# Performance work log

Measured on AMD Instinct MI355X. Metric: run time of the kernel, lower is better.

## Reference

```python
import jax, jax.numpy as jnp
import numpy as np


def setup_inputs() -> dict:
    key = jax.random.key(0)
    k1, k2, k3 = jax.random.split(key, 3)
    l, p, m, n = 8, 1, 4096, 1024
    inp = jax.random.normal(k1, (l, p, m, n), dtype=jnp.float32)
    alpha = jax.random.uniform(k2, (1,), dtype=jnp.float32, minval=0.001, maxval=1.0)
    beta = jax.random.uniform(k3, (1,), dtype=jnp.float32, minval=0.001, maxval=1.0)
    return {"input": inp, "alpha": alpha, "beta": beta}


def reference(input, alpha, beta):
    # w[0] = 1; w[k] = w[k-1] + alpha / w[k-1] - beta * input[..., k-1]
    l, p, m, n = input.shape
    a = alpha[0]
    b = beta[0]
    # scan over the last axis: move it to leading axis; only first n-1 inputs drive the recurrence
    xs = jnp.moveaxis(input[..., : n - 1], -1, 0)  # (n-1, l, p, m)
    w0 = jnp.ones((l, p, m), dtype=input.dtype)

    def step(w, x):
        w_next = w + a / w - b * x
        return w_next, w_next

    _, ws = jax.lax.scan(step, w0, xs)  # (n-1, l, p, m)
    wm = jnp.concatenate([w0[None], ws], axis=0)  # (n, l, p, m)
    wm = jnp.moveaxis(wm, 0, -1)  # (l, p, m, n)
    return wm.reshape(l, m * n)  # valid because p == 1
```

## Files before the change

### kernel.cpp

```cpp
#include <hip/hip_runtime.h>


#define N_COLS 1024
#define NCHUNK 64
#define KIN 6

#define WAITVM(n) asm volatile("s_waitcnt vmcnt(" #n ")" ::: "memory")
#define WAITLGKM0() asm volatile("s_waitcnt lgkmcnt(0)" ::: "memory")
#define BARRIER() __builtin_amdgcn_s_barrier()

__device__ __forceinline__ float fdiv_rn_exact(float a, float w) {
    float d, n, r0, e, r1, q, e2, q1, e3, f, res;
    unsigned long long sj;
    asm volatile(
        "v_div_scale_f32 %[d], vcc, %[w], %[w], %[a]\n\t"
        "v_div_scale_f32 %[n], %[sj], %[a], %[w], %[a]\n\t"
        "v_rcp_f32 %[r0], %[d]\n\t"
        "s_nop 1\n\t"
        "v_fma_f32 %[e], -%[d], %[r0], 1.0\n\t"
        "v_fma_f32 %[r1], %[e], %[r0], %[r0]\n\t"
        "v_mul_f32 %[q], %[n], %[r1]\n\t"
        "v_fma_f32 %[e2], -%[d], %[q], %[n]\n\t"
        "v_fma_f32 %[q1], %[e2], %[r1], %[q]\n\t"
        "v_fma_f32 %[e3], -%[d], %[q1], %[n]\n\t"
        "v_div_fmas_f32 %[f], %[e3], %[r1], %[q1]\n\t"
        "v_div_fixup_f32 %[res], %[f], %[w], %[a]"
        : [d] "=&v"(d), [n] "=&v"(n), [r0] "=&v"(r0), [e] "=&v"(e),
          [r1] "=&v"(r1), [q] "=&v"(q), [e2] "=&v"(e2), [q1] "=&v"(q1),
          [e3] "=&v"(e3), [f] "=&v"(f), [res] "=v"(res), [sj] "=&s"(sj)
        : [a] "v"(a), [w] "v"(w)
        : "vcc");
    return res;
}

__device__ __forceinline__ float stepf(float w, float x, float a, float b) {
    return __fsub_rn(__fadd_rn(w, fdiv_rn_exact(a, w)), __fmul_rn(b, x));
}

__global__ __launch_bounds__(256) void DDK_77644418777662_kernel(
    const float* __restrict__ in, float* __restrict__ out,
    const float* __restrict__ alpha, const float* __restrict__ beta,
    int n_rows) {
    __shared__ float ibuf[KIN * 2048];
    __shared__ float obuf[2 * 2048];

    const int tid = threadIdx.x;
    const int wid = tid >> 6;
    const int lane = tid & 63;
    const int row_base = blockIdx.x * 128;
    if (row_base >= n_rows) return;

    const int t = lane >> 2;
    const int u = lane & 3;
    const int cg = u ^ ((t >> 1) & 3);

    if (wid == 2) {
        const float* src0 = in + (size_t)(row_base + t) * N_COLS + cg * 4;

#define STAGE_AT(S, C) do {                                                    \
    float* dst_ = ibuf + (S) * 2048;                                           \
    const float* s_ = src0 + (size_t)(C) * 16;                                 \
    _Pragma("unroll")                                                          \
    for (int q_ = 0; q_ < 8; ++q_) {                                           \
        __builtin_amdgcn_global_load_lds(                                      \
            (const __attribute__((address_space(1))) void*)(s_ + q_ * 16 * N_COLS), \
            (__attribute__((address_space(3))) void*)(dst_ + q_ * 256), 16, 0, 0);  \
    }                                                                          \
} while (0)

        WAITVM(0);
        STAGE_AT(0, 0); STAGE_AT(1, 1); STAGE_AT(2, 2);
        STAGE_AT(3, 3); STAGE_AT(4, 4);
        WAITVM(32);

        int slot = KIN - 1;
#pragma unroll 1
        for (int c = 0; c < NCHUNK; ++c) {
            BARRIER();
            if (c <= NCHUNK - KIN) {
                STAGE_AT(slot, c + KIN - 1);
                WAITVM(32);
                if (++slot == KIN) slot = 0;
            } else if (c == 59) { WAITVM(24); }
            else if (c == 60) { WAITVM(16); }
            else if (c == 61) { WAITVM(8); }
            else if (c == 62) { WAITVM(0); }
        }
        BARRIER();
#undef STAGE_AT

    } else if (wid == 3) {
        float* dst0 = out + (size_t)(row_base + t) * N_COLS + cg * 4;

#define STORE_CHUNK(C) do {                                                    \
    const float* ob_ = obuf + ((C) & 1) * 2048;                                \
    float4 v_[8];                                                              \
    _Pragma("unroll")                                                          \
    for (int q_ = 0; q_ < 8; ++q_)                                             \
        v_[q_] = *(const float4*)(ob_ + q_ * 256 + lane * 4);                  \
    WAITLGKM0();                                                               \
    _Pragma("unroll")                                                          \
    for (int q_ = 0; q_ < 8; ++q_)                                             \
        *(float4*)(dst0 + (size_t)q_ * 16 * N_COLS + (size_t)(C) * 16) = v_[q_]; \
} while (0)

#pragma unroll 1
        for (int c = 0; c < NCHUNK; ++c) {
            BARRIER();
            if (c >= 1) STORE_CHUNK(c - 1);
        }
        BARRIER();
        STORE_CHUNK(NCHUNK - 1);
#undef STORE_CHUNK

    } else {
        const float a = alpha[0];
        const float b = beta[0];

        const int r = (wid << 6) + lane;
        const int rq = r >> 4, rr = r & 15;
        const int s = (rr >> 1) & 3;
        const int off0 = rq * 256 + (rr * 4 + (0 ^ s)) * 4;
        const int off1 = rq * 256 + (rr * 4 + (1 ^ s)) * 4;
        const int off2 = rq * 256 + (rr * 4 + (2 ^ s)) * 4;
        const int off3 = rq * 256 + (rr * 4 + (3 ^ s)) * 4;

        float w = 1.0f;
        int rslot = 0;
#pragma unroll 1
        for (int c = 0; c < NCHUNK; ++c) {
            BARRIER();
            const float* ib = ibuf + rslot * 2048;
            float4 xa = *(const float4*)(ib + off0);
            float4 xb = *(const float4*)(ib + off1);
            float4 xc = *(const float4*)(ib + off2);
            float4 xd = *(const float4*)(ib + off3);
            float x[16] = {xa.x, xa.y, xa.z, xa.w, xb.x, xb.y, xb.z, xb.w,
                           xc.x, xc.y, xc.z, xc.w, xd.x, xd.y, xd.z, xd.w};
            float o[16];
            o[0] = w;
#pragma unroll
            for (int i = 1; i < 16; ++i) { w = stepf(w, x[i - 1], a, b); o[i] = w; }
            w = stepf(w, x[15], a, b);

            float* ob = obuf + (c & 1) * 2048;
            *(float4*)(ob + off0) = make_float4(o[0], o[1], o[2], o[3]);
            *(float4*)(ob + off1) = make_float4(o[4], o[5], o[6], o[7]);
            *(float4*)(ob + off2) = make_float4(o[8], o[9], o[10], o[11]);
            *(float4*)(ob + off3) = make_float4(o[12], o[13], o[14], o[15]);
            WAITLGKM0();

            if (++rslot == KIN) rslot = 0;
        }
        BARRIER();
    }
}

extern "C" void kernel_launch(void* const* d_in, const int* in_sizes, int n_in,
                              void* d_out, int out_size, void* d_ws, size_t ws_size,
                              hipStream_t stream) {
    const float* in = (const float*)d_in[0];
    const float* alpha = (const float*)d_in[1];
    const float* beta = (const float*)d_in[2];
    float* out = (float*)d_out;

    int total = in_sizes[0];
    int n_rows = total / N_COLS;

    dim3 grid(n_rows / 128);
    dim3 block(256);
    DDK_77644418777662_kernel<<<grid, block, 0, stream>>>(in, out, alpha, beta,
                                                          n_rows);
}
```

Baseline: 283.3 us.

## Halve rows per block and double chunk width with an 8-deep input ring

Each block now covers 64 rows with a single compute wave (192 threads) in place of 128 rows with two compute waves. Chunks along the scan axis grow from 16 to 32 columns, so there are half as many barrier-synchronised iterations per block, and the input ring deepens from 6 to 8 slots with swizzled LDS offsets to match. The grid doubles, which raises block-level parallelism on a latency-bound serial recurrence. In exchange each compute lane does a longer dependent chain per chunk, and LDS use per block rises, which may limit how many blocks fit on a CU.

```diff
diff --git a/kernel.cpp b/kernel.cpp
--- a/kernel.cpp
+++ b/kernel.cpp
@@ -2,8 +2,11 @@
 
 
 #define N_COLS 1024
-#define NCHUNK 64
-#define KIN 6
+#define DC 32
+#define NDC 32
+#define RING 8
+#define ROWS 64
+#define SLOTF 2048
 
 #define WAITVM(n) asm volatile("s_waitcnt vmcnt(" #n ")" ::: "memory")
 #define WAITLGKM0() asm volatile("s_waitcnt lgkmcnt(0)" ::: "memory")
@@ -37,63 +40,62 @@
     return __fsub_rn(__fadd_rn(w, fdiv_rn_exact(a, w)), __fmul_rn(b, x));
 }
 
-__global__ __launch_bounds__(256) void DDK_77644418777662_kernel(
+__global__ __launch_bounds__(192) void DDK_77644418777662_kernel(
     const float* __restrict__ in, float* __restrict__ out,
     const float* __restrict__ alpha, const float* __restrict__ beta,
     int n_rows) {
-    __shared__ float ibuf[KIN * 2048];
-    __shared__ float obuf[2 * 2048];
+    __shared__ float ibuf[RING * SLOTF];
+    __shared__ float obuf[2 * SLOTF];
 
     const int tid = threadIdx.x;
     const int wid = tid >> 6;
     const int lane = tid & 63;
-    const int row_base = blockIdx.x * 128;
+    const int row_base = blockIdx.x * ROWS;
     if (row_base >= n_rows) return;
 
-    const int t = lane >> 2;
-    const int u = lane & 3;
-    const int cg = u ^ ((t >> 1) & 3);
+    const int lr = lane >> 3;
+    const int cg = (lane & 7) ^ lr;
 
-    if (wid == 2) {
-        const float* src0 = in + (size_t)(row_base + t) * N_COLS + cg * 4;
+    if (wid == 1) {
+        const float* src0 = in + (size_t)(row_base + lr) * N_COLS + cg * 4;
 
 #define STAGE_AT(S, C) do {                                                    \
-    float* dst_ = ibuf + (S) * 2048;                                           \
-    const float* s_ = src0 + (size_t)(C) * 16;                                 \
+    float* dst_ = ibuf + (S) * SLOTF;                                          \
+    const float* s_ = src0 + (C) * DC;                                         \
     _Pragma("unroll")                                                          \
     for (int q_ = 0; q_ < 8; ++q_) {                                           \
         __builtin_amdgcn_global_load_lds(                                      \
-            (const __attribute__((address_space(1))) void*)(s_ + q_ * 16 * N_COLS), \
-            (__attribute__((address_space(3))) void*)(dst_ + q_ * 256), 16, 0, 0);  \
+            (const __attribute__((address_space(1))) void*)(s_ + (size_t)q_ * 8 * N_COLS), \
+            (__attribute__((address_space(3))) void*)(dst_ + q_ * 256), 16, 0, 0);         \
     }                                                                          \
 } while (0)
 
         WAITVM(0);
-        STAGE_AT(0, 0); STAGE_AT(1, 1); STAGE_AT(2, 2);
-        STAGE_AT(3, 3); STAGE_AT(4, 4);
-        WAITVM(32);
+        STAGE_AT(0, 0); STAGE_AT(1, 1); STAGE_AT(2, 2); STAGE_AT(3, 3);
+        STAGE_AT(4, 4); STAGE_AT(5, 5); STAGE_AT(6, 6);
+        WAITVM(48);
 
-        int slot = KIN - 1;
 #pragma unroll 1
-        for (int c = 0; c < NCHUNK; ++c) {
+        for (int c = 0; c < NDC; ++c) {
             BARRIER();
-            if (c <= NCHUNK - KIN) {
-                STAGE_AT(slot, c + KIN - 1);
-                WAITVM(32);
-                if (++slot == KIN) slot = 0;
-            } else if (c == 59) { WAITVM(24); }
-            else if (c == 60) { WAITVM(16); }
-            else if (c == 61) { WAITVM(8); }
-            else if (c == 62) { WAITVM(0); }
+            if (c <= NDC - RING) {
+                STAGE_AT((c + 7) & 7, c + 7);
+                WAITVM(48);
+            } else if (c == 25) { WAITVM(40); }
+            else if (c == 26) { WAITVM(32); }
+            else if (c == 27) { WAITVM(24); }
+            else if (c == 28) { WAITVM(16); }
+            else if (c == 29) { WAITVM(8); }
+            else if (c == 30) { WAITVM(0); }
         }
         BARRIER();
 #undef STAGE_AT
 
-    } else if (wid == 3) {
-        float* dst0 = out + (size_t)(row_base + t) * N_COLS + cg * 4;
+    } else if (wid == 2) {
+        float* dst0 = out + (size_t)(row_base + lr) * N_COLS + cg * 4;
 
 #define STORE_CHUNK(C) do {                                                    \
-    const float* ob_ = obuf + ((C) & 1) * 2048;                                \
+    const float* ob_ = obuf + ((C) & 1) * SLOTF;                               \
     float4 v_[8];                                                              \
     _Pragma("unroll")                                                          \
     for (int q_ = 0; q_ < 8; ++q_)                                             \
@@ -101,56 +103,54 @@
     WAITLGKM0();                                                               \
     _Pragma("unroll")                                                          \
     for (int q_ = 0; q_ < 8; ++q_)                                             \
-        *(float4*)(dst0 + (size_t)q_ * 16 * N_COLS + (size_t)(C) * 16) = v_[q_]; \
+        *(float4*)(dst0 + (size_t)q_ * 8 * N_COLS + (C) * DC) = v_[q_];        \
 } while (0)
 
 #pragma unroll 1
-        for (int c = 0; c < NCHUNK; ++c) {
+        for (int c = 0; c < NDC; ++c) {
             BARRIER();
             if (c >= 1) STORE_CHUNK(c - 1);
         }
         BARRIER();
-        STORE_CHUNK(NCHUNK - 1);
+        STORE_CHUNK(NDC - 1);
 #undef STORE_CHUNK
 
     } else {
         const float a = alpha[0];
         const float b = beta[0];
 
-        const int r = (wid << 6) + lane;
-        const int rq = r >> 4, rr = r & 15;
-        const int s = (rr >> 1) & 3;
-        const int off0 = rq * 256 + (rr * 4 + (0 ^ s)) * 4;
-        const int off1 = rq * 256 + (rr * 4 + (1 ^ s)) * 4;
-        const int off2 = rq * 256 + (rr * 4 + (2 ^ s)) * 4;
-        const int off3 = rq * 256 + (rr * 4 + (3 ^ s)) * 4;
+        const int q = lane >> 3, h = lane & 7;
+        const int base_f = q * 256 + h * 32;
+        int off[8];
+#pragma unroll
+        for (int g = 0; g < 8; ++g) off[g] = base_f + ((g ^ h) * 4);
 
         float w = 1.0f;
-        int rslot = 0;
 #pragma unroll 1
-        for (int c = 0; c < NCHUNK; ++c) {
+        for (int c = 0; c < NDC; ++c) {
             BARRIER();
-            const float* ib = ibuf + rslot * 2048;
-            float4 xa = *(const float4*)(ib + off0);
-            float4 xb = *(const float4*)(ib + off1);
-            float4 xc = *(const float4*)(ib + off2);
-            float4 xd = *(const float4*)(ib + off3);
-            float x[16] = {xa.x, xa.y, xa.z, xa.w, xb.x, xb.y, xb.z, xb.w,
-                           xc.x, xc.y, xc.z, xc.w, xd.x, xd.y, xd.z, xd.w};
-            float o[16];
+            const float* ib = ibuf + (c & 7) * SLOTF;
+            float4 v[8];
+#pragma unroll
+            for (int g = 0; g < 8; ++g) v[g] = *(const float4*)(ib + off[g]);
+            float x[32];
+#pragma unroll
+            for (int g = 0; g < 8; ++g) {
+                x[g * 4 + 0] = v[g].x; x[g * 4 + 1] = v[g].y;
+                x[g * 4 + 2] = v[g].z; x[g * 4 + 3] = v[g].w;
+            }
+            float o[32];
             o[0] = w;
 #pragma unroll
-            for (int i = 1; i < 16; ++i) { w = stepf(w, x[i - 1], a, b); o[i] = w; }
-            w = stepf(w, x[15], a, b);
+            for (int i = 1; i < 32; ++i) { w = stepf(w, x[i - 1], a, b); o[i] = w; }
+            w = stepf(w, x[31], a, b);
 
-            float* ob = obuf + (c & 1) * 2048;
-            *(float4*)(ob + off0) = make_float4(o[0], o[1], o[2], o[3]);
-            *(float4*)(ob + off1) = make_float4(o[4], o[5], o[6], o[7]);
-            *(float4*)(ob + off2) = make_float4(o[8], o[9], o[10], o[11]);
-            *(float4*)(ob + off3) = make_float4(o[12], o[13], o[14], o[15]);
+            float* ob = obuf + (c & 1) * SLOTF;
+#pragma unroll
+            for (int g = 0; g < 8; ++g)
+                *(float4*)(ob + off[g]) = make_float4(o[g * 4 + 0], o[g * 4 + 1],
+                                                      o[g * 4 + 2], o[g * 4 + 3]);
             WAITLGKM0();
-
-            if (++rslot == KIN) rslot = 0;
         }
         BARRIER();
     }
@@ -167,8 +167,8 @@
     int total = in_sizes[0];
     int n_rows = total / N_COLS;
 
-    dim3 grid(n_rows / 128);
-    dim3 block(256);
+    dim3 grid(n_rows / ROWS);
+    dim3 block(192);
     DDK_77644418777662_kernel<<<grid, block, 0, stream>>>(in, out, alpha, beta,
                                                           n_rows);
 }
```

Result: faster. 271.0 us (-4.3%).
